# Performance work log

Hardware: AMD Instinct MI355X
Metric: run time of the kernel (lower is better)

The kernel has to match this reference:

```python
import jax, jax.numpy as jnp
import numpy as np

N_NODES = 50000
N_EDGES = 800000
C_IN = 128
HEADS = 4
C_HEAD = 32  # c_out // heads = 128 // 4
NEG_SLOPE = 0.2


def setup_inputs() -> dict:
    key = jax.random.key(0)
    k_x, k_e, k_w, k_as, k_ad, k_b = jax.random.split(key, 6)
    x = jax.random.normal(k_x, (N_NODES, C_IN), dtype=jnp.float32)
    edge_index = jax.random.randint(k_e, (2, N_EDGES), 0, N_NODES, dtype=jnp.int64)
    # xavier_uniform_ with gain=1.414 on lin.weight [H*C, C_IN] -> same bound for W [C_IN, H*C]
    bound = 1.414 * np.sqrt(6.0 / (C_IN + HEADS * C_HEAD))
    W = jax.random.uniform(k_w, (C_IN, HEADS * C_HEAD), minval=-bound, maxval=bound, dtype=jnp.float32)
    # glorot init for attention vectors (PyG default)
    ab = np.sqrt(6.0 / (1 + HEADS * C_HEAD))
    att_src = jax.random.uniform(k_as, (HEADS, C_HEAD), minval=-ab, maxval=ab, dtype=jnp.float32)
    att_dst = jax.random.uniform(k_ad, (HEADS, C_HEAD), minval=-ab, maxval=ab, dtype=jnp.float32)
    bias = jnp.zeros((HEADS * C_HEAD,), dtype=jnp.float32)
    return {"x": x, "edge_index": edge_index, "W": W,
            "att_src": att_src, "att_dst": att_dst, "bias": bias}


def reference(x, edge_index, W, att_src, att_dst, bias):
    N = x.shape[0]
    H, C = att_src.shape
    # Linear projection, per-head split: [N, H, C]
    xl = (x @ W).reshape(N, H, C)
    a_src = jnp.einsum('nhc,hc->nh', xl, att_src)  # [N, H]
    a_dst = jnp.einsum('nhc,hc->nh', xl, att_dst)  # [N, H]

    src, dst = edge_index[0], edge_index[1]
    loop = jnp.arange(N, dtype=edge_index.dtype)
    # GATConv(add_self_loops=True): remove existing self loops, then add one per node.
    src_f = jnp.concatenate([src, loop])  # [E+N]
    dst_f = jnp.concatenate([dst, loop])
    drop = jnp.concatenate([src == dst, jnp.zeros((N,), dtype=bool)])

    e = jax.nn.leaky_relu(a_src[src_f] + a_dst[dst_f], NEG_SLOPE)  # [E+N, H]
    e = jnp.where(drop[:, None], -jnp.inf, e)

    # segment softmax over edges sharing a destination (every node has a self loop -> max is finite)
    m = jax.ops.segment_max(e, dst_f, num_segments=N)          # [N, H]
    ex = jnp.exp(e - m[dst_f])                                  # [E+N, H]
    denom = jax.ops.segment_sum(ex, dst_f, num_segments=N)     # [N, H]
    alpha = ex / denom[dst_f]                                   # [E+N, H]

    msg = xl[src_f] * alpha[:, :, None]                         # [E+N, H, C]
    out = jax.ops.segment_sum(msg, dst_f, num_segments=N)      # [N, H, C]
    out = out.reshape(N, H * C) + bias
    return out / jnp.sqrt(jnp.asarray(H, dtype=out.dtype))
```

## Files before the change

kernel.cpp:

```cpp
#include <hip/hip_runtime.h>
#include <math.h>

#define CDIM 128
#define HEADS 4
#define NEG 0.2f
#define BSTRIDE 64

typedef __attribute__((ext_vector_type(8))) short bf16x8;
typedef __attribute__((ext_vector_type(8))) unsigned short u16x8;
typedef __attribute__((ext_vector_type(4))) float f32x4;

static __device__ __forceinline__ unsigned short f2bf(float f) {
    unsigned u = __float_as_uint(f);
    u += 0x7FFFu + ((u >> 16) & 1u);
    return (unsigned short)(u >> 16);
}
static __device__ __forceinline__ float bf2f(unsigned short s) {
    return __uint_as_float((unsigned)s << 16);
}

#define LDS_STRIDE 136

__global__ __launch_bounds__(256) void wt_kernel(const float* __restrict__ W,
                                                 unsigned short* __restrict__ WT,
                                                 int* __restrict__ counts, int nClr) {
    int f = blockIdx.x * 256 + threadIdx.x;
    for (int i = f; i < nClr; i += 4096) counts[i] = 0;
    int k = f >> 5, c4 = (f & 31) * 4;
    float4 v = *(const float4*)(W + (size_t)k * CDIM + c4);
    WT[(size_t)(c4 + 0) * CDIM + k] = f2bf(v.x);
    WT[(size_t)(c4 + 1) * CDIM + k] = f2bf(v.y);
    WT[(size_t)(c4 + 2) * CDIM + k] = f2bf(v.z);
    WT[(size_t)(c4 + 3) * CDIM + k] = f2bf(v.w);
}

__global__ __launch_bounds__(256) void gemm_hist_kernel(const float* __restrict__ x,
                                                        const unsigned short* __restrict__ WT,
                                                        const float* __restrict__ att_src,
                                                        const float* __restrict__ att_dst,
                                                        unsigned short* __restrict__ xlh,
                                                        float* __restrict__ a_src,
                                                        float* __restrict__ a_dst, int N,
                                                        const int* __restrict__ esrc,
                                                        const int* __restrict__ edst,
                                                        int* __restrict__ counts,
                                                        unsigned* __restrict__ packed, int E,
                                                        int gemmBlocks) {
    __shared__ unsigned short As[64 * LDS_STRIDE];

    if ((int)blockIdx.x >= gemmBlocks) {
        int e = (blockIdx.x - gemmBlocks) * 256 + threadIdx.x;
        if (e < E) {
            int s = esrc[e], d = edst[e];
            unsigned pk = ~0u;
            if (s != d) {
                int r = atomicAdd(&counts[d], 1);
                pk = (unsigned)d | ((unsigned)r << 16);
            }
            packed[e] = pk;
        }
        return;
    }

    const int tid = threadIdx.x;
    const int row0 = blockIdx.x * 64;

#pragma unroll
    for (int i = 0; i < 8; ++i) {
        int f = tid + i * 256;
        int r = f >> 5, k4 = f & 31;
        float4 v = make_float4(0.f, 0.f, 0.f, 0.f);
        int gr = row0 + r;
        if (gr < N) v = *(const float4*)(x + (size_t)gr * CDIM + k4 * 4);
        ushort4 h;
        h.x = f2bf(v.x); h.y = f2bf(v.y); h.z = f2bf(v.z); h.w = f2bf(v.w);
        *(ushort4*)(&As[r * LDS_STRIDE + k4 * 4]) = h;
    }
    __syncthreads();

    const int wave = tid >> 6;
    const int lane = tid & 63;
    const int m    = lane & 15;
    const int quad = lane >> 4;
    const int wrow = wave * 16;

    bf16x8 a[4];
#pragma unroll
    for (int ks = 0; ks < 4; ++ks)
        a[ks] = *(const bf16x8*)(&As[(wrow + m) * LDS_STRIDE + ks * 32 + quad * 8]);

    f32x4 acc[8];
#pragma unroll
    for (int t = 0; t < 8; ++t) {
        f32x4 c = {0.f, 0.f, 0.f, 0.f};
#pragma unroll
        for (int ks = 0; ks < 4; ++ks) {
            bf16x8 b = *(const bf16x8*)(WT + (size_t)(t * 16 + m) * CDIM + ks * 32 + quad * 8);
            c = __builtin_amdgcn_mfma_f32_16x16x32_bf16(a[ks], b, c, 0, 0, 0);
        }
        acc[t] = c;
    }

    __syncthreads();
#pragma unroll
    for (int t = 0; t < 8; ++t)
#pragma unroll
        for (int reg = 0; reg < 4; ++reg)
            As[(wrow + quad * 4 + reg) * LDS_STRIDE + t * 16 + m] = f2bf(acc[t][reg]);
    __syncthreads();
    {
        int r = tid >> 2;
        int c = (tid & 3) * 32;
        int grow = row0 + r;
        if (grow < N) {
            u16x8 v0 = *(const u16x8*)(&As[r * LDS_STRIDE + c]);
            u16x8 v1 = *(const u16x8*)(&As[r * LDS_STRIDE + c + 8]);
            u16x8 v2 = *(const u16x8*)(&As[r * LDS_STRIDE + c + 16]);
            u16x8 v3 = *(const u16x8*)(&As[r * LDS_STRIDE + c + 24]);
            *(u16x8*)(xlh + (size_t)grow * CDIM + c)      = v0;
            *(u16x8*)(xlh + (size_t)grow * CDIM + c + 8)  = v1;
            *(u16x8*)(xlh + (size_t)grow * CDIM + c + 16) = v2;
            *(u16x8*)(xlh + (size_t)grow * CDIM + c + 24) = v3;
        }
    }

    float ps[4][4], pd[4][4];
#pragma unroll
    for (int h = 0; h < 4; ++h)
#pragma unroll
        for (int reg = 0; reg < 4; ++reg) { ps[h][reg] = 0.f; pd[h][reg] = 0.f; }
#pragma unroll
    for (int t = 0; t < 8; ++t) {
        int h = t >> 1;
        float vs = att_src[t * 16 + m];
        float vd = att_dst[t * 16 + m];
#pragma unroll
        for (int reg = 0; reg < 4; ++reg) {
            ps[h][reg] += acc[t][reg] * vs;
            pd[h][reg] += acc[t][reg] * vd;
        }
    }
#pragma unroll
    for (int off = 8; off > 0; off >>= 1) {
#pragma unroll
        for (int h = 0; h < 4; ++h)
#pragma unroll
            for (int reg = 0; reg < 4; ++reg) {
                ps[h][reg] += __shfl_down(ps[h][reg], off, 16);
                pd[h][reg] += __shfl_down(pd[h][reg], off, 16);
            }
    }
    if (m == 0) {
#pragma unroll
        for (int reg = 0; reg < 4; ++reg) {
            int row = row0 + wrow + quad * 4 + reg;
            if (row < N) {
#pragma unroll
                for (int h = 0; h < 4; ++h) {
                    a_src[row * 4 + h] = ps[h][reg];
                    a_dst[row * 4 + h] = pd[h][reg];
                }
            }
        }
    }
}

__global__ __launch_bounds__(256) void scatter_kernel(const int* __restrict__ src,
                                                      const unsigned* __restrict__ packed,
                                                      int* __restrict__ bucket, int E) {
    int base = (blockIdx.x * 256 + threadIdx.x) * 2;
    if (base + 2 <= E) {
        int2 s2 = *(const int2*)(src + base);
        uint2 p2 = *(const uint2*)(packed + base);
        unsigned r0 = p2.x >> 16, r1 = p2.y >> 16;
        if (p2.x != ~0u && r0 < BSTRIDE) bucket[(p2.x & 0xFFFFu) * BSTRIDE + r0] = s2.x;
        if (p2.y != ~0u && r1 < BSTRIDE) bucket[(p2.y & 0xFFFFu) * BSTRIDE + r1] = s2.y;
    } else if (base < E) {
        unsigned pk = packed[base];
        unsigned r = pk >> 16;
        if (pk != ~0u && r < BSTRIDE) bucket[(pk & 0xFFFFu) * BSTRIDE + r] = src[base];
    }
}

__global__ __launch_bounds__(256) void gather_kernel(const int* __restrict__ counts,
                                                     const int* __restrict__ bucket,
                                                     const unsigned short* __restrict__ xlh,
                                                     const float* __restrict__ a_src,
                                                     const float* __restrict__ a_dst,
                                                     const float* __restrict__ bias,
                                                     float* __restrict__ out, int N) {
    const int node = blockIdx.x * 4 + (threadIdx.x >> 6);
    const int lane = threadIdx.x & 63;
    const int g = lane >> 4;
    const int lane16 = lane & 15;
    if (node >= N) return;
    const int c8 = lane16 * 8;
    const int h = lane16 >> 2;

    const float ad = a_dst[node * 4 + h];
    const int beg = node * BSTRIDE;
    int cnt = counts[node];
    if (cnt > BSTRIDE) cnt = BSTRIDE;

    float acc[8];
#pragma unroll
    for (int i = 0; i < 8; ++i) acc[i] = 0.f;
    float den = 0.f;

    int j = g;
    for (; j + 12 < cnt; j += 16) {
        int s[4];
#pragma unroll
        for (int q = 0; q < 4; ++q) s[q] = bucket[beg + j + 4 * q];
        float e[4];
#pragma unroll
        for (int q = 0; q < 4; ++q) e[q] = a_src[s[q] * 4 + h] + ad;
        u16x8 u[4];
#pragma unroll
        for (int q = 0; q < 4; ++q) u[q] = *(const u16x8*)(xlh + (size_t)s[q] * CDIM + c8);
        float w[4];
#pragma unroll
        for (int q = 0; q < 4; ++q) {
            float eq = e[q] > 0.f ? e[q] : NEG * e[q];
            w[q] = __expf(eq);
        }
#pragma unroll
        for (int q = 0; q < 4; ++q) {
#pragma unroll
            for (int i = 0; i < 8; ++i) acc[i] += w[q] * bf2f(u[q][i]);
            den += w[q];
        }
    }
    for (; j < cnt; j += 4) {
        int s = bucket[beg + j];
        float e = a_src[s * 4 + h] + ad;
        u16x8 u = *(const u16x8*)(xlh + (size_t)s * CDIM + c8);
        e = e > 0.f ? e : NEG * e;
        float w = __expf(e);
#pragma unroll
        for (int i = 0; i < 8; ++i) acc[i] += w * bf2f(u[i]);
        den += w;
    }
    if (g == 0) {
        float es = a_src[node * 4 + h] + ad;
        es = es > 0.f ? es : NEG * es;
        float ws = __expf(es);
        u16x8 u = *(const u16x8*)(xlh + (size_t)node * CDIM + c8);
#pragma unroll
        for (int i = 0; i < 8; ++i) acc[i] += ws * bf2f(u[i]);
        den += ws;
    }
#pragma unroll
    for (int i = 0; i < 8; ++i) {
        acc[i] += __shfl_xor(acc[i], 16);
        acc[i] += __shfl_xor(acc[i], 32);
    }
    den += __shfl_xor(den, 16);
    den += __shfl_xor(den, 32);

    if (g == 0) {
        float inv = 1.0f / den;
        float4 b0 = *(const float4*)(bias + c8);
        float4 b1 = *(const float4*)(bias + c8 + 4);
        float4 o0, o1;
        o0.x = (acc[0] * inv + b0.x) * 0.5f;
        o0.y = (acc[1] * inv + b0.y) * 0.5f;
        o0.z = (acc[2] * inv + b0.z) * 0.5f;
        o0.w = (acc[3] * inv + b0.w) * 0.5f;
        o1.x = (acc[4] * inv + b1.x) * 0.5f;
        o1.y = (acc[5] * inv + b1.y) * 0.5f;
        o1.z = (acc[6] * inv + b1.z) * 0.5f;
        o1.w = (acc[7] * inv + b1.w) * 0.5f;
        *(float4*)(out + (size_t)node * CDIM + c8) = o0;
        *(float4*)(out + (size_t)node * CDIM + c8 + 4) = o1;
    }
}

extern "C" void kernel_launch(void* const* d_in, const int* in_sizes, int n_in,
                              void* d_out, int out_size, void* d_ws, size_t ws_size,
                              hipStream_t stream) {
    const float* x       = (const float*)d_in[0];
    const int*   ei      = (const int*)d_in[1];
    const float* W       = (const float*)d_in[2];
    const float* att_src = (const float*)d_in[3];
    const float* att_dst = (const float*)d_in[4];
    const float* bias    = (const float*)d_in[5];
    float* out = (float*)d_out;

    const int N = in_sizes[0] / CDIM;
    const int E = in_sizes[1] / 2;

    char* wsb = (char*)d_ws;
    unsigned short* xlh = (unsigned short*)wsb;         wsb += (size_t)N * CDIM * sizeof(unsigned short);
    unsigned short* WT  = (unsigned short*)wsb;         wsb += (size_t)CDIM * CDIM * sizeof(unsigned short);
    float* a_src = (float*)wsb;                         wsb += (size_t)N * HEADS * sizeof(float);
    float* a_dst = (float*)wsb;                         wsb += (size_t)N * HEADS * sizeof(float);
    int* counts  = (int*)wsb;                           wsb += (size_t)N * sizeof(int);
    unsigned* packed = (unsigned*)wsb;                  wsb += (size_t)E * sizeof(unsigned);
    int* bucket  = (int*)wsb;                           wsb += (size_t)N * BSTRIDE * sizeof(int);

    wt_kernel<<<16, 256, 0, stream>>>(W, WT, counts, N);
    const int gemmBlocks = (N + 63) / 64;
    const int histBlocks = (E + 255) / 256;
    gemm_hist_kernel<<<gemmBlocks + histBlocks, 256, 0, stream>>>(
        x, WT, att_src, att_dst, xlh, a_src, a_dst, N, ei, ei + E, counts, packed, E, gemmBlocks);
    scatter_kernel<<<((E + 1) / 2 + 255) / 256, 256, 0, stream>>>(ei, packed, bucket, E);
    gather_kernel<<<(N + 3) / 4, 256, 0, stream>>>(counts, bucket, xlh, a_src, a_dst, bias, out, N);
}
```

Measured before the change: 174.8 us.

## Store GEMM output directly, widen scatter to 4 edges, use explicit bf16 FMA unpack

The GEMM epilogue no longer stages the bf16 projection through LDS with two barriers; each lane writes its 2-byte outputs straight to global memory, which saves barriers but produces scattered narrow stores. The scatter kernel now handles four edges per thread with int4/uint4 loads instead of two. The gather accumulation unpacks bf16 pairs from 32-bit words and uses explicit fmaf to cut conversion instructions.

```diff
diff --git a/kernel.cpp b/kernel.cpp
--- a/kernel.cpp
+++ b/kernel.cpp
@@ -17,6 +17,16 @@
 }
 static __device__ __forceinline__ float bf2f(unsigned short s) {
     return __uint_as_float((unsigned)s << 16);
+}
+
+static __device__ __forceinline__ void accum8(float* acc, float w, u16x8 u) {
+    const unsigned* pw = (const unsigned*)&u;
+#pragma unroll
+    for (int i = 0; i < 4; ++i) {
+        unsigned wd = pw[i];
+        acc[2 * i]     = fmaf(w, __uint_as_float(wd << 16), acc[2 * i]);
+        acc[2 * i + 1] = fmaf(w, __uint_as_float(wd & 0xFFFF0000u), acc[2 * i + 1]);
+    }
 }
 
 #define LDS_STRIDE 136
@@ -101,26 +111,12 @@
         acc[t] = c;
     }
 
-    __syncthreads();
-#pragma unroll
-    for (int t = 0; t < 8; ++t)
-#pragma unroll
-        for (int reg = 0; reg < 4; ++reg)
-            As[(wrow + quad * 4 + reg) * LDS_STRIDE + t * 16 + m] = f2bf(acc[t][reg]);
-    __syncthreads();
-    {
-        int r = tid >> 2;
-        int c = (tid & 3) * 32;
-        int grow = row0 + r;
-        if (grow < N) {
-            u16x8 v0 = *(const u16x8*)(&As[r * LDS_STRIDE + c]);
-            u16x8 v1 = *(const u16x8*)(&As[r * LDS_STRIDE + c + 8]);
-            u16x8 v2 = *(const u16x8*)(&As[r * LDS_STRIDE + c + 16]);
-            u16x8 v3 = *(const u16x8*)(&As[r * LDS_STRIDE + c + 24]);
-            *(u16x8*)(xlh + (size_t)grow * CDIM + c)      = v0;
-            *(u16x8*)(xlh + (size_t)grow * CDIM + c + 8)  = v1;
-            *(u16x8*)(xlh + (size_t)grow * CDIM + c + 16) = v2;
-            *(u16x8*)(xlh + (size_t)grow * CDIM + c + 24) = v3;
+#pragma unroll
+    for (int t = 0; t < 8; ++t) {
+#pragma unroll
+        for (int reg = 0; reg < 4; ++reg) {
+            int row = row0 + wrow + quad * 4 + reg;
+            if (row < N) xlh[(size_t)row * CDIM + t * 16 + m] = f2bf(acc[t][reg]);
         }
     }
 
@@ -168,17 +164,24 @@
 __global__ __launch_bounds__(256) void scatter_kernel(const int* __restrict__ src,
                                                       const unsigned* __restrict__ packed,
                                                       int* __restrict__ bucket, int E) {
-    int base = (blockIdx.x * 256 + threadIdx.x) * 2;
-    if (base + 2 <= E) {
-        int2 s2 = *(const int2*)(src + base);
-        uint2 p2 = *(const uint2*)(packed + base);
-        unsigned r0 = p2.x >> 16, r1 = p2.y >> 16;
-        if (p2.x != ~0u && r0 < BSTRIDE) bucket[(p2.x & 0xFFFFu) * BSTRIDE + r0] = s2.x;
-        if (p2.y != ~0u && r1 < BSTRIDE) bucket[(p2.y & 0xFFFFu) * BSTRIDE + r1] = s2.y;
-    } else if (base < E) {
-        unsigned pk = packed[base];
-        unsigned r = pk >> 16;
-        if (pk != ~0u && r < BSTRIDE) bucket[(pk & 0xFFFFu) * BSTRIDE + r] = src[base];
+    int base = (blockIdx.x * 256 + threadIdx.x) * 4;
+    if (base + 4 <= E) {
+        int4 s4 = *(const int4*)(src + base);
+        uint4 p4 = *(const uint4*)(packed + base);
+        int ss[4] = {s4.x, s4.y, s4.z, s4.w};
+        unsigned pp[4] = {p4.x, p4.y, p4.z, p4.w};
+#pragma unroll
+        for (int q = 0; q < 4; ++q) {
+            unsigned r = pp[q] >> 16;
+            if (pp[q] != ~0u && r < BSTRIDE)
+                bucket[(pp[q] & 0xFFFFu) * BSTRIDE + r] = ss[q];
+        }
+    } else {
+        for (int e = base; e < E; ++e) {
+            unsigned pk = packed[e];
+            unsigned r = pk >> 16;
+            if (pk != ~0u && r < BSTRIDE) bucket[(pk & 0xFFFFu) * BSTRIDE + r] = src[e];
+        }
     }
 }
 
@@ -226,8 +229,7 @@
         }
 #pragma unroll
         for (int q = 0; q < 4; ++q) {
-#pragma unroll
-            for (int i = 0; i < 8; ++i) acc[i] += w[q] * bf2f(u[q][i]);
+            accum8(acc, w[q], u[q]);
             den += w[q];
         }
     }
@@ -237,8 +239,7 @@
         u16x8 u = *(const u16x8*)(xlh + (size_t)s * CDIM + c8);
         e = e > 0.f ? e : NEG * e;
         float w = __expf(e);
-#pragma unroll
-        for (int i = 0; i < 8; ++i) acc[i] += w * bf2f(u[i]);
+        accum8(acc, w, u);
         den += w;
     }
     if (g == 0) {
@@ -246,8 +247,7 @@
         es = es > 0.f ? es : NEG * es;
         float ws = __expf(es);
         u16x8 u = *(const u16x8*)(xlh + (size_t)node * CDIM + c8);
-#pragma unroll
-        for (int i = 0; i < 8; ++i) acc[i] += ws * bf2f(u[i]);
+        accum8(acc, ws, u);
         den += ws;
     }
 #pragma unroll
@@ -304,6 +304,6 @@
     const int histBlocks = (E + 255) / 256;
     gemm_hist_kernel<<<gemmBlocks + histBlocks, 256, 0, stream>>>(
         x, WT, att_src, att_dst, xlh, a_src, a_dst, N, ei, ei + E, counts, packed, E, gemmBlocks);
-    scatter_kernel<<<((E + 1) / 2 + 255) / 256, 256, 0, stream>>>(ei, packed, bucket, E);
+    scatter_kernel<<<((E + 3) / 4 + 255) / 256, 256, 0, stream>>>(ei, packed, bucket, E);
     gather_kernel<<<(N + 3) / 4, 256, 0, stream>>>(counts, bucket, xlh, a_src, a_dst, bias, out, N);
 }
```

After: 169.8 us (median of 2 runs). -2.8%, faster.
